# Kernel optimization log

Measured on AMD Instinct MI355X. Metric: run time of the kernel, lower is better.

Reference implementation:

```python
import jax, jax.numpy as jnp
import numpy as np
import math

NEIGHBOR_RADIUS = 30.0

def _masked_softmax(logits, mask, axis):
    # mask: bool, True = keep; all-masked rows return zeros
    p = jax.nn.softmax(jnp.where(mask, logits, -1e9), axis=axis) * mask.astype(logits.dtype)
    return p / jnp.clip(jnp.sum(p, axis=axis, keepdims=True), 1e-9, None)

def _forward(agents_state, agents_mask, map_polylines, map_poly_mask,
             map_poly_type, map_tl_status, map_on_route,
             pm_w1, pm_b1, pm_w2, pm_b2, type_emb, tl_emb, route_emb,
             mo_w1, mo_b1, mo_w2, mo_b2,
             ae_w1, ae_b1, ae_w2, ae_b2, ae_w3, ae_b3,
             mr_w1, mr_b1, mr_w2, mr_b2,
             nr_w1, nr_b1, nr_w2, nr_b2,
             to_w1, to_b1, to_w2, to_b2):
    relu = jax.nn.relu
    a_mask = (agents_mask > 0.5).astype(agents_state.dtype)   # (B,N,T)
    a_feat = agents_state[..., :5]
    # ---- map polyline node encoder ----
    h = relu(map_polylines @ pm_w1 + pm_b1)                   # (B,M,L,H)
    h = relu(h @ pm_w2 + pm_b2)
    h = h.max(axis=2)                                         # (B,M,H) max-pool over points
    t_idx = jnp.clip(map_poly_type, 0, type_emb.shape[0] - 1)
    s_idx = jnp.clip(map_tl_status, 0, tl_emb.shape[0] - 1)
    r_idx = jnp.clip(map_on_route, 0, route_emb.shape[0] - 1)
    h = h + type_emb[t_idx] + tl_emb[s_idx] + route_emb[r_idx]
    h = relu(h @ mo_w1 + mo_b1) @ mo_w2 + mo_b2
    map_mask = map_poly_mask > 0.5                            # (B,M) bool
    map_node = h * map_mask[..., None].astype(h.dtype)        # (B,M,D)
    map_center = map_polylines.mean(axis=2)                   # (B,M,2)
    # ---- agent state encoder ----
    a = relu(a_feat @ ae_w1 + ae_b1)
    a = relu(a @ ae_w2 + ae_b2)
    a_emb = (a @ ae_w3 + ae_b3) * a_mask[..., None]           # (B,N,T,D)
    D = a_emb.shape[-1]
    # ---- agent -> map attention ----
    agent_pos = a_feat[..., 0:2]
    rel = map_center[:, None, None, :, :] - agent_pos[:, :, :, None, :]  # (B,N,T,M,2)
    dist = jnp.linalg.norm(rel, axis=-1, keepdims=True)
    rel_feat = jnp.concatenate([rel, dist], axis=-1)          # (B,N,T,M,3)
    rel_score = (relu(rel_feat @ mr_w1 + mr_b1) @ mr_w2 + mr_b2)[..., 0]  # (B,N,T,M)
    dot = jnp.einsum('bntd,bmd->bntm', a_emb, map_node) / math.sqrt(D)
    score_mask = jnp.broadcast_to(map_mask[:, None, None, :], dot.shape)
    attn = _masked_softmax(dot + rel_score, score_mask, axis=-1)
    map_ctx = jnp.einsum('bntm,bmd->bntd', attn, map_node)    # (B,N,T,D)
    # ---- neighbor graph attention ----
    pos = a_feat[..., 0:2]
    vel = a_feat[..., 3:5]
    pos_j = jnp.transpose(pos, (0, 2, 1, 3))                  # (B,T,N,2)
    vel_j = jnp.transpose(vel, (0, 2, 1, 3))
    rel_pos = pos_j[:, None, :, :, :] - pos[:, :, :, None, :] # (B,N,T,N,2) = p_j - p_i
    rel_vel = vel_j[:, None, :, :, :] - vel[:, :, :, None, :]
    dist_ij = jnp.linalg.norm(rel_pos, axis=-1, keepdims=True)
    rel_ij = jnp.concatenate([rel_pos, rel_vel, dist_ij], axis=-1)        # (B,N,T,N,5)
    nbr_score = (relu(rel_ij @ nr_w1 + nr_b1) @ nr_w2 + nr_b2)[..., 0]    # (B,N,T,N)
    am_b = agents_mask > 0.5
    valid_i = am_b[..., None]                                 # (B,N,T,1)
    valid_j = jnp.transpose(am_b, (0, 2, 1))[:, None, :, :]   # (B,1,T,N)
    N = pos.shape[1]
    not_self = ~jnp.eye(N, dtype=bool)[None, :, None, :]      # (1,N,1,N)
    nbr_mask = valid_i & valid_j & (dist_ij[..., 0] <= NEIGHBOR_RADIUS) & not_self
    dot_n = jnp.einsum('bitd,bjtd->bitj', a_emb, a_emb) / math.sqrt(D)
    w_n = _masked_softmax(dot_n + nbr_score, nbr_mask, axis=-1)
    nbr_ctx = jnp.einsum('bitj,bjtd->bitd', w_n, a_emb)       # (B,N,T,D)
    # ---- tau head ----
    tau = jnp.concatenate([a_emb, map_ctx, nbr_ctx], axis=-1)
    tau = relu(tau @ to_w1 + to_b1) @ to_w2 + to_b2
    return tau * a_mask[..., None]

def setup_inputs() -> dict:
    key = jax.random.key(0)
    B, N, T, M, L = 2, 32, 32, 256, 20
    H, D, TAU = 128, 128, 64
    ks = jax.random.split(key, 32)
    def f(i, shp):
        return jax.random.normal(ks[i], shp, jnp.float32) * 0.05
    inp = {}
    inp['agents_state'] = jax.random.normal(ks[0], (B, N, T, 5), jnp.float32) * jnp.array([50., 50., 1., 5., 5.], jnp.float32)
    inp['agents_mask'] = jnp.ones((B, N, T), jnp.float32)
    inp['map_polylines'] = jax.random.normal(ks[1], (B, M, L, 2), jnp.float32) * 50.0
    inp['map_poly_mask'] = jnp.ones((B, M), jnp.float32)
    inp['map_poly_type'] = jax.random.randint(ks[2], (B, M), 0, 4)
    inp['map_tl_status'] = jax.random.randint(ks[3], (B, M), 0, 8)
    inp['map_on_route'] = jax.random.randint(ks[4], (B, M), 0, 2)
    inp['pm_w1'] = f(5, (2, H));  inp['pm_b1'] = jnp.zeros((H,), jnp.float32)
    inp['pm_w2'] = f(6, (H, H)); inp['pm_b2'] = jnp.zeros((H,), jnp.float32)
    inp['type_emb'] = f(7, (4, H)); inp['tl_emb'] = f(8, (8, H)); inp['route_emb'] = f(9, (2, H))
    inp['mo_w1'] = f(10, (H, H)); inp['mo_b1'] = jnp.zeros((H,), jnp.float32)
    inp['mo_w2'] = f(11, (H, D)); inp['mo_b2'] = jnp.zeros((D,), jnp.float32)
    inp['ae_w1'] = f(12, (5, H)); inp['ae_b1'] = jnp.zeros((H,), jnp.float32)
    inp['ae_w2'] = f(13, (H, H)); inp['ae_b2'] = jnp.zeros((H,), jnp.float32)
    inp['ae_w3'] = f(14, (H, D)); inp['ae_b3'] = jnp.zeros((D,), jnp.float32)
    inp['mr_w1'] = f(15, (3, H)); inp['mr_b1'] = jnp.zeros((H,), jnp.float32)
    inp['mr_w2'] = f(16, (H, 1)); inp['mr_b2'] = jnp.zeros((1,), jnp.float32)
    inp['nr_w1'] = f(17, (5, H)); inp['nr_b1'] = jnp.zeros((H,), jnp.float32)
    inp['nr_w2'] = f(18, (H, 1)); inp['nr_b2'] = jnp.zeros((1,), jnp.float32)
    inp['to_w1'] = f(19, (3 * D, H)); inp['to_b1'] = jnp.zeros((H,), jnp.float32)
    inp['to_w2'] = f(20, (H, TAU)); inp['to_b2'] = jnp.zeros((TAU,), jnp.float32)
    return inp

def reference(agents_state, agents_mask, map_polylines, map_poly_mask,
              map_poly_type, map_tl_status, map_on_route,
              pm_w1, pm_b1, pm_w2, pm_b2, type_emb, tl_emb, route_emb,
              mo_w1, mo_b1, mo_w2, mo_b2,
              ae_w1, ae_b1, ae_w2, ae_b2, ae_w3, ae_b3,
              mr_w1, mr_b1, mr_w2, mr_b2,
              nr_w1, nr_b1, nr_w2, nr_b2,
              to_w1, to_b1, to_w2, to_b2):
    return _forward(agents_state, agents_mask, map_polylines, map_poly_mask,
                    map_poly_type, map_tl_status, map_on_route,
                    pm_w1, pm_b1, pm_w2, pm_b2, type_emb, tl_emb, route_emb,
                    mo_w1, mo_b1, mo_w2, mo_b2,
                    ae_w1, ae_b1, ae_w2, ae_b2, ae_w3, ae_b3,
                    mr_w1, mr_b1, mr_w2, mr_b2,
                    nr_w1, nr_b1, nr_w2, nr_b2,
                    to_w1, to_b1, to_w2, to_b2)
```

## Files before the change

kernel.cpp:

```cpp
#include <hip/hip_runtime.h>

#define RSQRT_D 0.08838834764831843f

__global__ __launch_bounds__(256) void kAB_front(
    const float* __restrict__ poly, const float* __restrict__ pmask,
    const int* __restrict__ ptype, const int* __restrict__ ptl, const int* __restrict__ proute,
    const float* __restrict__ pm_w1, const float* __restrict__ pm_b1,
    const float* __restrict__ pm_w2, const float* __restrict__ pm_b2,
    const float* __restrict__ type_emb, const float* __restrict__ tl_emb, const float* __restrict__ route_emb,
    const float* __restrict__ mo_w1, const float* __restrict__ mo_b1,
    const float* __restrict__ mo_w2, const float* __restrict__ mo_b2,
    const float* __restrict__ astate, const float* __restrict__ amask,
    const float* __restrict__ ae_w1, const float* __restrict__ ae_b1,
    const float* __restrict__ ae_w2, const float* __restrict__ ae_b2,
    const float* __restrict__ ae_w3, const float* __restrict__ ae_b3,
    float* __restrict__ map_node, float* __restrict__ map_nodeT, float* __restrict__ center,
    float* __restrict__ a_emb, float* __restrict__ aT, float* __restrict__ posT)
{
    int tid = threadIdx.x;
    if (blockIdx.x < 512) {
        int bm = blockIdx.x;
        int b = bm >> 8, m = bm & 255;
        int h = tid & 127, rw = tid >> 7;
        __shared__ float xch[2][128];
        __shared__ __align__(16) float hvs[128];
        __shared__ __align__(16) float g2[128];
        __shared__ __align__(16) float h1s[2][128][12];

        {
            int k = h;
            int half = rw;
            const float* pp = poly + bm*40 + half*20;
            float wx = pm_w1[k], wy = pm_w1[128+k], bb = pm_b1[k];
            float h1v[10];
            #pragma unroll
            for (int u = 0; u < 10; ++u) {
                float x = pp[2*u], y = pp[2*u+1];
                h1v[u] = fmaxf(fmaf(wx, x, fmaf(wy, y, bb)), 0.f);
            }
            float4 s0 = make_float4(h1v[0], h1v[1], h1v[2], h1v[3]);
            float4 s1 = make_float4(h1v[4], h1v[5], h1v[6], h1v[7]);
            float2 s2 = make_float2(h1v[8], h1v[9]);
            *(float4*)&h1s[half][k][0] = s0;
            *(float4*)&h1s[half][k][4] = s1;
            *(float2*)&h1s[half][k][8] = s2;
        }
        __syncthreads();

        float acc[10];
        #pragma unroll
        for (int u = 0; u < 10; ++u) acc[u] = 0.f;
        const float* w2p = pm_w2 + h;
        #pragma unroll 2
        for (int k = 0; k < 128; ++k) {
            float w2v = w2p[k*128];
            float4 A  = *(const float4*)&h1s[rw][k][0];
            float4 Bv = *(const float4*)&h1s[rw][k][4];
            float2 Cv = *(const float2*)&h1s[rw][k][8];
            acc[0] = fmaf(A.x,  w2v, acc[0]);
            acc[1] = fmaf(A.y,  w2v, acc[1]);
            acc[2] = fmaf(A.z,  w2v, acc[2]);
            acc[3] = fmaf(A.w,  w2v, acc[3]);
            acc[4] = fmaf(Bv.x, w2v, acc[4]);
            acc[5] = fmaf(Bv.y, w2v, acc[5]);
            acc[6] = fmaf(Bv.z, w2v, acc[6]);
            acc[7] = fmaf(Bv.w, w2v, acc[7]);
            acc[8] = fmaf(Cv.x, w2v, acc[8]);
            acc[9] = fmaf(Cv.y, w2v, acc[9]);
        }
        float mx = acc[0];
        #pragma unroll
        for (int u = 1; u < 10; ++u) mx = fmaxf(mx, acc[u]);
        xch[rw][h] = mx;
        __syncthreads();
        if (rw == 0) {
            float v = fmaxf(fmaxf(mx, xch[1][h]) + pm_b2[h], 0.f);
            int ti = min(max(ptype[bm],0),3);
            int si = min(max(ptl[bm],0),7);
            int ri = min(max(proute[bm],0),1);
            hvs[h] = v + type_emb[ti*128+h] + tl_emb[si*128+h] + route_emb[ri*128+h];
        }
        __syncthreads();
        {
            float a1 = (rw == 0) ? mo_b1[h] : 0.f;
            int k0 = rw * 64;
            for (int kc = 0; kc < 16; ++kc) {
                float4 xv = *(const float4*)&hvs[k0 + kc*4];
                a1 = fmaf(xv.x, mo_w1[(k0+kc*4+0)*128+h],
                     fmaf(xv.y, mo_w1[(k0+kc*4+1)*128+h],
                     fmaf(xv.z, mo_w1[(k0+kc*4+2)*128+h],
                     fmaf(xv.w, mo_w1[(k0+kc*4+3)*128+h], a1))));
            }
            xch[rw][h] = a1;
        }
        __syncthreads();
        if (tid < 128) g2[tid] = fmaxf(xch[0][tid] + xch[1][tid], 0.f);
        __syncthreads();
        {
            float a2 = (rw == 0) ? mo_b2[h] : 0.f;
            int k0 = rw * 64;
            for (int kc = 0; kc < 16; ++kc) {
                float4 xv = *(const float4*)&g2[k0 + kc*4];
                a2 = fmaf(xv.x, mo_w2[(k0+kc*4+0)*128+h],
                     fmaf(xv.y, mo_w2[(k0+kc*4+1)*128+h],
                     fmaf(xv.z, mo_w2[(k0+kc*4+2)*128+h],
                     fmaf(xv.w, mo_w2[(k0+kc*4+3)*128+h], a2))));
            }
            xch[rw][h] = a2;
        }
        __syncthreads();
        if (tid < 128) {
            float a2 = xch[0][tid] + xch[1][tid];
            float mk = (pmask[bm] > 0.5f) ? 1.f : 0.f;
            a2 *= mk;
            map_node[bm*128 + tid] = a2;
            map_nodeT[(b*128+tid)*256 + m] = a2;
        }
        if (tid == 0) {
            float sx = 0.f, sy = 0.f;
            #pragma unroll
            for (int l = 0; l < 20; ++l) { sx += poly[bm*40 + 2*l]; sy += poly[bm*40 + 2*l + 1]; }
            center[bm*2+0] = sx * 0.05f;
            center[bm*2+1] = sy * 0.05f;
        }
    } else {
        int h = tid & 127, rp = tid >> 7;
        int r0 = (blockIdx.x - 512)*8 + rp*4;
        __shared__ float f5[2][4][5];
        __shared__ __align__(16) float a1s[2][4][128];
        if (h < 20) f5[rp][h/5][h%5] = astate[(r0 + h/5)*5 + (h%5)];
        __syncthreads();
        float b1v = ae_b1[h];
        float v[4];
        {
            float w0 = ae_w1[h], w1 = ae_w1[128+h], w2 = ae_w1[256+h], w3 = ae_w1[384+h], w4 = ae_w1[512+h];
            #pragma unroll
            for (int r = 0; r < 4; ++r) {
                float a = b1v;
                a = fmaf(f5[rp][r][0], w0, a); a = fmaf(f5[rp][r][1], w1, a);
                a = fmaf(f5[rp][r][2], w2, a); a = fmaf(f5[rp][r][3], w3, a);
                a = fmaf(f5[rp][r][4], w4, a);
                v[r] = fmaxf(a, 0.f);
            }
        }
        #pragma unroll
        for (int r = 0; r < 4; ++r) a1s[rp][r][h] = v[r];
        __syncthreads();
        {
            float b2v = ae_b2[h];
            float a0 = b2v, a1 = b2v, a2 = b2v, a3 = b2v;
            for (int kc = 0; kc < 32; ++kc) {
                float4 x0 = *(const float4*)&a1s[rp][0][kc*4];
                float4 x1 = *(const float4*)&a1s[rp][1][kc*4];
                float4 x2 = *(const float4*)&a1s[rp][2][kc*4];
                float4 x3 = *(const float4*)&a1s[rp][3][kc*4];
                float w0 = ae_w2[(kc*4+0)*128+h], w1 = ae_w2[(kc*4+1)*128+h];
                float w2 = ae_w2[(kc*4+2)*128+h], w3 = ae_w2[(kc*4+3)*128+h];
                a0 = fmaf(x0.x,w0,fmaf(x0.y,w1,fmaf(x0.z,w2,fmaf(x0.w,w3,a0))));
                a1 = fmaf(x1.x,w0,fmaf(x1.y,w1,fmaf(x1.z,w2,fmaf(x1.w,w3,a1))));
                a2 = fmaf(x2.x,w0,fmaf(x2.y,w1,fmaf(x2.z,w2,fmaf(x2.w,w3,a2))));
                a3 = fmaf(x3.x,w0,fmaf(x3.y,w1,fmaf(x3.z,w2,fmaf(x3.w,w3,a3))));
            }
            v[0]=fmaxf(a0,0.f); v[1]=fmaxf(a1,0.f); v[2]=fmaxf(a2,0.f); v[3]=fmaxf(a3,0.f);
        }
        __syncthreads();
        #pragma unroll
        for (int r = 0; r < 4; ++r) a1s[rp][r][h] = v[r];
        __syncthreads();
        {
            float b3v = ae_b3[h];
            float a0 = b3v, a1 = b3v, a2 = b3v, a3 = b3v;
            for (int kc = 0; kc < 32; ++kc) {
                float4 x0 = *(const float4*)&a1s[rp][0][kc*4];
                float4 x1 = *(const float4*)&a1s[rp][1][kc*4];
                float4 x2 = *(const float4*)&a1s[rp][2][kc*4];
                float4 x3 = *(const float4*)&a1s[rp][3][kc*4];
                float w0 = ae_w3[(kc*4+0)*128+h], w1 = ae_w3[(kc*4+1)*128+h];
                float w2 = ae_w3[(kc*4+2)*128+h], w3 = ae_w3[(kc*4+3)*128+h];
                a0 = fmaf(x0.x,w0,fmaf(x0.y,w1,fmaf(x0.z,w2,fmaf(x0.w,w3,a0))));
                a1 = fmaf(x1.x,w0,fmaf(x1.y,w1,fmaf(x1.z,w2,fmaf(x1.w,w3,a1))));
                a2 = fmaf(x2.x,w0,fmaf(x2.y,w1,fmaf(x2.z,w2,fmaf(x2.w,w3,a2))));
                a3 = fmaf(x3.x,w0,fmaf(x3.y,w1,fmaf(x3.z,w2,fmaf(x3.w,w3,a3))));
            }
            v[0]=a0; v[1]=a1; v[2]=a2; v[3]=a3;
        }
        #pragma unroll
        for (int r = 0; r < 4; ++r) {
            int rr = r0 + r;
            float mk = (amask[rr] > 0.5f) ? 1.f : 0.f;
            float e = v[r] * mk;
            a_emb[rr*128 + h] = e;
            int bb = rr >> 10, nn = (rr >> 5) & 31, tt = rr & 31;
            int bt = bb*32 + tt;
            aT[(bt*128 + h)*32 + nn] = e;
        }
        if (h < 20) {
            int r = h / 5, c = h % 5;
            int rr = r0 + r;
            int bb = rr >> 10, nn = (rr >> 5) & 31, tt = rr & 31;
            int bt = bb*32 + tt;
            float val;
            if      (c == 0) val = f5[rp][r][0];
            else if (c == 1) val = f5[rp][r][1];
            else if (c == 2) val = f5[rp][r][3];
            else if (c == 3) val = f5[rp][r][4];
            else             val = amask[rr];
            posT[(bt*5 + c)*32 + nn] = val;
        }
    }
}

__global__ __launch_bounds__(512) void kCD_fused(
    const float* __restrict__ astate, const float* __restrict__ amask,
    const float* __restrict__ pmask,
    const float* __restrict__ a_emb, const float* __restrict__ map_node,
    const float* __restrict__ map_nodeT, const float* __restrict__ center,
    const float* __restrict__ mr_w1, const float* __restrict__ mr_b1,
    const float* __restrict__ mr_w2, const float* __restrict__ mr_b2,
    const float* __restrict__ aT, const float* __restrict__ posT,
    const float* __restrict__ nr_w1, const float* __restrict__ nr_b1,
    const float* __restrict__ nr_w2, const float* __restrict__ nr_b2,
    const float* __restrict__ to_w1, const float* __restrict__ to_b1,
    const float* __restrict__ to_w2, const float* __restrict__ to_b2,
    float* __restrict__ out)
{
    int tid = threadIdx.x;
    int r0 = blockIdx.x * 4;
    int b = r0 >> 10, t0 = r0 & 31;

    __shared__ float lg4[4][256];
    __shared__ __align__(16) float p4[256*4];
    __shared__ float ctxp[4][128];
    __shared__ float pj[4][32];
    __shared__ __align__(16) float tau[4][384];
    __shared__ float redn[4][128];
    __shared__ __align__(16) float gpart[4][4][128];
    __shared__ __align__(16) float g1s[4][128];

    if (tid < 256) {
        int m = tid;
        float rx[4], ry[4], dd[4], dt[4], sA[4];
        float b2c = mr_b2[0];
        float cx = center[(b*256+m)*2+0], cy = center[(b*256+m)*2+1];
        #pragma unroll
        for (int r = 0; r < 4; ++r) {
            float px = astate[(r0+r)*5+0], py = astate[(r0+r)*5+1];
            rx[r] = cx - px; ry[r] = cy - py;
            dd[r] = sqrtf(rx[r]*rx[r] + ry[r]*ry[r]);
            dt[r] = 0.f; sA[r] = b2c;
        }
        const float* mT = map_nodeT + b*128*256 + m;
        const float* ae0 = a_emb + (size_t)(r0+0)*128;
        const float* ae1 = a_emb + (size_t)(r0+1)*128;
        const float* ae2 = a_emb + (size_t)(r0+2)*128;
        const float* ae3 = a_emb + (size_t)(r0+3)*128;
        #pragma unroll 4
        for (int hh = 0; hh < 128; ++hh) {
            float wa = mr_w1[hh], wb = mr_w1[128+hh], wc = mr_w1[256+hh];
            float bb = mr_b1[hh], w2 = mr_w2[hh];
            float v = mT[hh*256];
            float t10 = fmaf(rx[0], wa, fmaf(ry[0], wb, fmaf(dd[0], wc, bb)));
            float t11 = fmaf(rx[1], wa, fmaf(ry[1], wb, fmaf(dd[1], wc, bb)));
            float t12 = fmaf(rx[2], wa, fmaf(ry[2], wb, fmaf(dd[2], wc, bb)));
            float t13 = fmaf(rx[3], wa, fmaf(ry[3], wb, fmaf(dd[3], wc, bb)));
            sA[0] = fmaf(fmaxf(t10, 0.f), w2, sA[0]);
            sA[1] = fmaf(fmaxf(t11, 0.f), w2, sA[1]);
            sA[2] = fmaf(fmaxf(t12, 0.f), w2, sA[2]);
            sA[3] = fmaf(fmaxf(t13, 0.f), w2, sA[3]);
            dt[0] = fmaf(v, ae0[hh], dt[0]);
            dt[1] = fmaf(v, ae1[hh], dt[1]);
            dt[2] = fmaf(v, ae2[hh], dt[2]);
            dt[3] = fmaf(v, ae3[hh], dt[3]);
        }
        bool mk = pmask[b*256+m] > 0.5f;
        #pragma unroll
        for (int r = 0; r < 4; ++r)
            lg4[r][m] = mk ? fmaf(dt[r], RSQRT_D, sA[r]) : -1e30f;
    } else {
        int lam = tid & 63, wv = (tid >> 6) & 3;
        int r = r0 + wv;
        int ii = (r >> 5) & 31, tt = r & 31;
        int bt = b*32 + tt;
        int j = lam & 31, hs = lam >> 5;
        float pxi = astate[r*5+0], pyi = astate[r*5+1], vxi = astate[r*5+3], vyi = astate[r*5+4];
        const float* pT = posT + bt*160;
        float pxj = pT[j], pyj = pT[32+j], vxj = pT[64+j], vyj = pT[96+j], mj = pT[128+j];
        float rpx = pxj-pxi, rpy = pyj-pyi, rvx = vxj-vxi, rvy = vyj-vyi;
        float ddv = sqrtf(rpx*rpx + rpy*rpy);
        const float* ei = a_emb + (size_t)r*128;
        const float* aTp = aT + (size_t)bt*4096 + j;
        float s = 0.f, dot = 0.f;
        int h0 = hs*64;
        #pragma unroll 8
        for (int q = 0; q < 64; ++q) {
            int hh = h0 + q;
            float wA = nr_w1[hh], wB = nr_w1[128+hh], wC = nr_w1[256+hh];
            float wD = nr_w1[384+hh], wE = nr_w1[512+hh];
            float bb = nr_b1[hh], w2 = nr_w2[hh];
            float t1 = fmaf(rpx, wA, fmaf(rpy, wB, fmaf(rvx, wC,
                       fmaf(rvy, wD, fmaf(ddv, wE, bb)))));
            s = fmaf(fmaxf(t1, 0.f), w2, s);
            dot = fmaf(ei[hh], aTp[hh*32], dot);
        }
        s   += __shfl_xor(s, 32);
        dot += __shfl_xor(dot, 32);
        bool vi = amask[r] > 0.5f, vj = mj > 0.5f;
        bool ok = vi && vj && (ddv <= 30.0f) && (j != ii);
        float lg = ok ? fmaf(dot, RSQRT_D, s + nr_b2[0]) : -1e30f;
        float mxv = lg;
        #pragma unroll
        for (int off = 16; off; off >>= 1) mxv = fmaxf(mxv, __shfl_xor(mxv, off));
        float e = (lg > -1e29f) ? expf(lg - mxv) : 0.f;
        float sm = e;
        #pragma unroll
        for (int off = 16; off; off >>= 1) sm += __shfl_xor(sm, off);
        if (hs == 0) pj[wv][j] = e / fmaxf(sm, 1e-9f);
    }
    __syncthreads();

    if (tid < 256) {
        int lam = tid & 63, wv = tid >> 6;
        float x0 = lg4[wv][lam], x1 = lg4[wv][64+lam], x2 = lg4[wv][128+lam], x3 = lg4[wv][192+lam];
        float mxv = fmaxf(fmaxf(x0,x1), fmaxf(x2,x3));
        #pragma unroll
        for (int off = 32; off; off >>= 1) mxv = fmaxf(mxv, __shfl_xor(mxv, off));
        float e0 = (x0 > -1e29f) ? expf(x0-mxv) : 0.f;
        float e1 = (x1 > -1e29f) ? expf(x1-mxv) : 0.f;
        float e2 = (x2 > -1e29f) ? expf(x2-mxv) : 0.f;
        float e3 = (x3 > -1e29f) ? expf(x3-mxv) : 0.f;
        float sm = e0+e1+e2+e3;
        #pragma unroll
        for (int off = 32; off; off >>= 1) sm += __shfl_xor(sm, off);
        float inv = 1.f / fmaxf(sm, 1e-9f);
        p4[lam*4 + wv]       = e0*inv;
        p4[(64+lam)*4 + wv]  = e1*inv;
        p4[(128+lam)*4 + wv] = e2*inv;
        p4[(192+lam)*4 + wv] = e3*inv;
    } else {
        int idx = tid - 256;
        int d = idx & 127, rr = idx >> 7;
        tau[rr][d]   = a_emb[(size_t)(r0+rr)*128 + d];
        tau[rr+2][d] = a_emb[(size_t)(r0+rr+2)*128 + d];
    }
    __syncthreads();

    float pv0 = 0.f, pv1 = 0.f, pv2 = 0.f, pv3 = 0.f;
    float na0 = 0.f, na1 = 0.f, na2 = 0.f, na3 = 0.f;
    if (tid < 256) {
        int d = tid & 127, hf = tid >> 7;
        const float* mn = map_node + (b*256 + hf*128)*128 + d;
        const float4* ppv = (const float4*)p4 + hf*128;
        #pragma unroll 4
        for (int mm = 0; mm < 128; ++mm) {
            float4 pvv = ppv[mm];
            float v = mn[mm*128];
            pv0 = fmaf(pvv.x, v, pv0); pv1 = fmaf(pvv.y, v, pv1);
            pv2 = fmaf(pvv.z, v, pv2); pv3 = fmaf(pvv.w, v, pv3);
        }
        if (hf == 1) { ctxp[0][d]=pv0; ctxp[1][d]=pv1; ctxp[2][d]=pv2; ctxp[3][d]=pv3; }
    } else {
        int local = tid - 256;
        int d = local & 127, hf = local >> 7;
        for (int jj = 0; jj < 16; ++jj) {
            int j2 = hf*16 + jj;
            float p0 = pj[0][j2], p1 = pj[1][j2], p2 = pj[2][j2], p3 = pj[3][j2];
            const float* ejb = a_emb + (size_t)((b*32 + j2)*32 + t0)*128 + d;
            na0 = fmaf(p0, ejb[0],   na0);
            na1 = fmaf(p1, ejb[128], na1);
            na2 = fmaf(p2, ejb[256], na2);
            na3 = fmaf(p3, ejb[384], na3);
        }
        if (hf == 1) { redn[0][d]=na0; redn[1][d]=na1; redn[2][d]=na2; redn[3][d]=na3; }
    }
    __syncthreads();

    if (tid < 128) {
        int d = tid;
        tau[0][128+d] = pv0 + ctxp[0][d];
        tau[1][128+d] = pv1 + ctxp[1][d];
        tau[2][128+d] = pv2 + ctxp[2][d];
        tau[3][128+d] = pv3 + ctxp[3][d];
    } else if (tid >= 256 && tid < 384) {
        int d = tid - 256;
        tau[0][256+d] = na0 + redn[0][d];
        tau[1][256+d] = na1 + redn[1][d];
        tau[2][256+d] = na2 + redn[2][d];
        tau[3][256+d] = na3 + redn[3][d];
    }
    __syncthreads();

    {
        int h6 = tid & 63, kq = (tid >> 6) & 3, side = tid >> 8;
        int col = side*64 + h6;
        float a0v = 0.f, a1v = 0.f, a2v = 0.f, a3v = 0.f;
        for (int c = 0; c < 24; ++c) {
            int k4 = kq*24 + c;
            float4 x0 = *(const float4*)&tau[0][k4*4];
            float4 x1 = *(const float4*)&tau[1][k4*4];
            float4 x2 = *(const float4*)&tau[2][k4*4];
            float4 x3 = *(const float4*)&tau[3][k4*4];
            float w0 = to_w1[(k4*4+0)*128 + col];
            float w1 = to_w1[(k4*4+1)*128 + col];
            float w2 = to_w1[(k4*4+2)*128 + col];
            float w3 = to_w1[(k4*4+3)*128 + col];
            a0v = fmaf(x0.x,w0,fmaf(x0.y,w1,fmaf(x0.z,w2,fmaf(x0.w,w3,a0v))));
            a1v = fmaf(x1.x,w0,fmaf(x1.y,w1,fmaf(x1.z,w2,fmaf(x1.w,w3,a1v))));
            a2v = fmaf(x2.x,w0,fmaf(x2.y,w1,fmaf(x2.z,w2,fmaf(x2.w,w3,a2v))));
            a3v = fmaf(x3.x,w0,fmaf(x3.y,w1,fmaf(x3.z,w2,fmaf(x3.w,w3,a3v))));
        }
        gpart[kq][0][col] = a0v;
        gpart[kq][1][col] = a1v;
        gpart[kq][2][col] = a2v;
        gpart[kq][3][col] = a3v;
    }
    __syncthreads();

    {
        int h = tid & 127, rr = tid >> 7;
        float s = gpart[0][rr][h] + gpart[1][rr][h] + gpart[2][rr][h] + gpart[3][rr][h];
        g1s[rr][h] = fmaxf(s + to_b1[h], 0.f);
    }
    __syncthreads();

    if (tid < 256) {
        int o = tid & 63, row = tid >> 6;
        float a2 = to_b2[o];
        for (int kc = 0; kc < 32; ++kc) {
            float4 g = *(const float4*)&g1s[row][kc*4];
            a2 = fmaf(g.x, to_w2[(kc*4+0)*64 + o],
                 fmaf(g.y, to_w2[(kc*4+1)*64 + o],
                 fmaf(g.z, to_w2[(kc*4+2)*64 + o],
                 fmaf(g.w, to_w2[(kc*4+3)*64 + o], a2))));
        }
        float mk = (amask[r0+row] > 0.5f) ? 1.f : 0.f;
        out[(r0+row)*64 + o] = a2 * mk;
    }
}

extern "C" void kernel_launch(void* const* d_in, const int* in_sizes, int n_in,
                              void* d_out, int out_size, void* d_ws, size_t ws_size,
                              hipStream_t stream) {
    const float* agents_state  = (const float*)d_in[0];
    const float* agents_mask   = (const float*)d_in[1];
    const float* map_polylines = (const float*)d_in[2];
    const float* map_poly_mask = (const float*)d_in[3];
    const int*   map_poly_type = (const int*)d_in[4];
    const int*   map_tl_status = (const int*)d_in[5];
    const int*   map_on_route  = (const int*)d_in[6];
    const float* pm_w1 = (const float*)d_in[7];
    const float* pm_b1 = (const float*)d_in[8];
    const float* pm_w2 = (const float*)d_in[9];
    const float* pm_b2 = (const float*)d_in[10];
    const float* type_emb  = (const float*)d_in[11];
    const float* tl_emb    = (const float*)d_in[12];
    const float* route_emb = (const float*)d_in[13];
    const float* mo_w1 = (const float*)d_in[14];
    const float* mo_b1 = (const float*)d_in[15];
    const float* mo_w2 = (const float*)d_in[16];
    const float* mo_b2 = (const float*)d_in[17];
    const float* ae_w1 = (const float*)d_in[18];
    const float* ae_b1 = (const float*)d_in[19];
    const float* ae_w2 = (const float*)d_in[20];
    const float* ae_b2 = (const float*)d_in[21];
    const float* ae_w3 = (const float*)d_in[22];
    const float* ae_b3 = (const float*)d_in[23];
    const float* mr_w1 = (const float*)d_in[24];
    const float* mr_b1 = (const float*)d_in[25];
    const float* mr_w2 = (const float*)d_in[26];
    const float* mr_b2 = (const float*)d_in[27];
    const float* nr_w1 = (const float*)d_in[28];
    const float* nr_b1 = (const float*)d_in[29];
    const float* nr_w2 = (const float*)d_in[30];
    const float* nr_b2 = (const float*)d_in[31];
    const float* to_w1 = (const float*)d_in[32];
    const float* to_b1 = (const float*)d_in[33];
    const float* to_w2 = (const float*)d_in[34];
    const float* to_b2 = (const float*)d_in[35];

    float* ws = (float*)d_ws;
    float* map_node  = ws;
    float* map_nodeT = ws + 65536;
    float* center    = ws + 131072;
    float* a_emb     = ws + 132096;
    float* aT        = ws + 394240;
    float* posT      = ws + 656384;

    float* out = (float*)d_out;

    kAB_front<<<768, 256, 0, stream>>>(map_polylines, map_poly_mask,
        map_poly_type, map_tl_status, map_on_route,
        pm_w1, pm_b1, pm_w2, pm_b2, type_emb, tl_emb, route_emb,
        mo_w1, mo_b1, mo_w2, mo_b2,
        agents_state, agents_mask,
        ae_w1, ae_b1, ae_w2, ae_b2, ae_w3, ae_b3,
        map_node, map_nodeT, center, a_emb, aT, posT);

    kCD_fused<<<512, 512, 0, stream>>>(agents_state, agents_mask, map_poly_mask,
        a_emb, map_node, map_nodeT, center,
        mr_w1, mr_b1, mr_w2, mr_b2,
        aT, posT,
        nr_w1, nr_b1, nr_w2, nr_b2,
        to_w1, to_b1, to_w2, to_b2,
        out);
}
```

Before: 179.5 us.

## Halve rows per block in fused attention kernel and split map-score reduction

Each block of the fused agent-map/agent-agent/output kernel now handles 2 rows instead of 4, and the grid is doubled to 1024 blocks. The map-logit loop over 128 hidden units is split across two thread halves, whose partial sums are combined through shared memory. The a_emb load is moved into the otherwise idle threads of the first phase, and launch bounds now request 8 waves per SIMD. This raises parallelism and occupancy, at the cost of weight reuse across rows, so to_w1, map_node and the MLP weights are re-read twice as often.

```diff
diff --git a/kernel.cpp b/kernel.cpp
--- a/kernel.cpp
+++ b/kernel.cpp
@@ -210,7 +210,7 @@
     }
 }
 
-__global__ __launch_bounds__(512) void kCD_fused(
+__global__ __launch_bounds__(512, 8) void kCD_fused(
     const float* __restrict__ astate, const float* __restrict__ amask,
     const float* __restrict__ pmask,
     const float* __restrict__ a_emb, const float* __restrict__ map_node,
@@ -225,59 +225,61 @@
     float* __restrict__ out)
 {
     int tid = threadIdx.x;
-    int r0 = blockIdx.x * 4;
+    int r0 = blockIdx.x * 2;
     int b = r0 >> 10, t0 = r0 & 31;
 
-    __shared__ float lg4[4][256];
-    __shared__ __align__(16) float p4[256*4];
-    __shared__ float ctxp[4][128];
-    __shared__ float pj[4][32];
-    __shared__ __align__(16) float tau[4][384];
-    __shared__ float redn[4][128];
-    __shared__ __align__(16) float gpart[4][4][128];
-    __shared__ __align__(16) float g1s[4][128];
-
-    if (tid < 256) {
-        int m = tid;
-        float rx[4], ry[4], dd[4], dt[4], sA[4];
+    __shared__ float lg4[2][256];
+    __shared__ __align__(16) float p4[256*2];
+    __shared__ float sp1[2][256];
+    __shared__ float dp1[2][256];
+    __shared__ float ctxp[2][128];
+    __shared__ float pj[2][32];
+    __shared__ __align__(16) float tau[2][384];
+    __shared__ float redn[2][128];
+    __shared__ __align__(16) float gpart[4][2][128];
+    __shared__ __align__(16) float g1s[2][128];
+
+    float sA0, sA1, dt0, dt1;
+    {
+        int m = tid & 255, kh = tid >> 8;
         float b2c = mr_b2[0];
         float cx = center[(b*256+m)*2+0], cy = center[(b*256+m)*2+1];
-        #pragma unroll
-        for (int r = 0; r < 4; ++r) {
-            float px = astate[(r0+r)*5+0], py = astate[(r0+r)*5+1];
-            rx[r] = cx - px; ry[r] = cy - py;
-            dd[r] = sqrtf(rx[r]*rx[r] + ry[r]*ry[r]);
-            dt[r] = 0.f; sA[r] = b2c;
-        }
+        float px0 = astate[(r0+0)*5+0], py0 = astate[(r0+0)*5+1];
+        float px1 = astate[(r0+1)*5+0], py1 = astate[(r0+1)*5+1];
+        float rx0 = cx - px0, ry0 = cy - py0;
+        float rx1 = cx - px1, ry1 = cy - py1;
+        float dd0 = sqrtf(rx0*rx0 + ry0*ry0);
+        float dd1 = sqrtf(rx1*rx1 + ry1*ry1);
+        sA0 = kh ? 0.f : b2c; sA1 = sA0;
+        dt0 = 0.f; dt1 = 0.f;
         const float* mT = map_nodeT + b*128*256 + m;
         const float* ae0 = a_emb + (size_t)(r0+0)*128;
         const float* ae1 = a_emb + (size_t)(r0+1)*128;
-        const float* ae2 = a_emb + (size_t)(r0+2)*128;
-        const float* ae3 = a_emb + (size_t)(r0+3)*128;
+        int h0 = kh*64;
         #pragma unroll 4
-        for (int hh = 0; hh < 128; ++hh) {
+        for (int q = 0; q < 64; ++q) {
+            int hh = h0 + q;
             float wa = mr_w1[hh], wb = mr_w1[128+hh], wc = mr_w1[256+hh];
             float bb = mr_b1[hh], w2 = mr_w2[hh];
             float v = mT[hh*256];
-            float t10 = fmaf(rx[0], wa, fmaf(ry[0], wb, fmaf(dd[0], wc, bb)));
-            float t11 = fmaf(rx[1], wa, fmaf(ry[1], wb, fmaf(dd[1], wc, bb)));
-            float t12 = fmaf(rx[2], wa, fmaf(ry[2], wb, fmaf(dd[2], wc, bb)));
-            float t13 = fmaf(rx[3], wa, fmaf(ry[3], wb, fmaf(dd[3], wc, bb)));
-            sA[0] = fmaf(fmaxf(t10, 0.f), w2, sA[0]);
-            sA[1] = fmaf(fmaxf(t11, 0.f), w2, sA[1]);
-            sA[2] = fmaf(fmaxf(t12, 0.f), w2, sA[2]);
-            sA[3] = fmaf(fmaxf(t13, 0.f), w2, sA[3]);
-            dt[0] = fmaf(v, ae0[hh], dt[0]);
-            dt[1] = fmaf(v, ae1[hh], dt[1]);
-            dt[2] = fmaf(v, ae2[hh], dt[2]);
-            dt[3] = fmaf(v, ae3[hh], dt[3]);
-        }
+            float t10 = fmaf(rx0, wa, fmaf(ry0, wb, fmaf(dd0, wc, bb)));
+            float t11 = fmaf(rx1, wa, fmaf(ry1, wb, fmaf(dd1, wc, bb)));
+            sA0 = fmaf(fmaxf(t10, 0.f), w2, sA0);
+            sA1 = fmaf(fmaxf(t11, 0.f), w2, sA1);
+            dt0 = fmaf(v, ae0[hh], dt0);
+            dt1 = fmaf(v, ae1[hh], dt1);
+        }
+        if (kh) { sp1[0][m] = sA0; sp1[1][m] = sA1; dp1[0][m] = dt0; dp1[1][m] = dt1; }
+    }
+    __syncthreads();
+
+    if (tid < 256) {
+        int m = tid;
         bool mk = pmask[b*256+m] > 0.5f;
-        #pragma unroll
-        for (int r = 0; r < 4; ++r)
-            lg4[r][m] = mk ? fmaf(dt[r], RSQRT_D, sA[r]) : -1e30f;
-    } else {
-        int lam = tid & 63, wv = (tid >> 6) & 3;
+        lg4[0][m] = mk ? fmaf(dt0 + dp1[0][m], RSQRT_D, sA0 + sp1[0][m]) : -1e30f;
+        lg4[1][m] = mk ? fmaf(dt1 + dp1[1][m], RSQRT_D, sA1 + sp1[1][m]) : -1e30f;
+    } else if (tid < 384) {
+        int lam = tid & 63, wv = (tid >> 6) & 1;
         int r = r0 + wv;
         int ii = (r >> 5) & 31, tt = r & 31;
         int bt = b*32 + tt;
@@ -315,10 +317,14 @@
         #pragma unroll
         for (int off = 16; off; off >>= 1) sm += __shfl_xor(sm, off);
         if (hs == 0) pj[wv][j] = e / fmaxf(sm, 1e-9f);
-    }
-    __syncthreads();
-
-    if (tid < 256) {
+    } else {
+        int d = tid & 127;
+        tau[0][d] = a_emb[(size_t)r0*128 + d];
+        tau[1][d] = a_emb[(size_t)(r0+1)*128 + d];
+    }
+    __syncthreads();
+
+    if (tid < 128) {
         int lam = tid & 63, wv = tid >> 6;
         float x0 = lg4[wv][lam], x1 = lg4[wv][64+lam], x2 = lg4[wv][128+lam], x3 = lg4[wv][192+lam];
         float mxv = fmaxf(fmaxf(x0,x1), fmaxf(x2,x3));
@@ -332,45 +338,37 @@
         #pragma unroll
         for (int off = 32; off; off >>= 1) sm += __shfl_xor(sm, off);
         float inv = 1.f / fmaxf(sm, 1e-9f);
-        p4[lam*4 + wv]       = e0*inv;
-        p4[(64+lam)*4 + wv]  = e1*inv;
-        p4[(128+lam)*4 + wv] = e2*inv;
-        p4[(192+lam)*4 + wv] = e3*inv;
-    } else {
-        int idx = tid - 256;
-        int d = idx & 127, rr = idx >> 7;
-        tau[rr][d]   = a_emb[(size_t)(r0+rr)*128 + d];
-        tau[rr+2][d] = a_emb[(size_t)(r0+rr+2)*128 + d];
-    }
-    __syncthreads();
-
-    float pv0 = 0.f, pv1 = 0.f, pv2 = 0.f, pv3 = 0.f;
-    float na0 = 0.f, na1 = 0.f, na2 = 0.f, na3 = 0.f;
+        p4[lam*2 + wv]       = e0*inv;
+        p4[(64+lam)*2 + wv]  = e1*inv;
+        p4[(128+lam)*2 + wv] = e2*inv;
+        p4[(192+lam)*2 + wv] = e3*inv;
+    }
+    __syncthreads();
+
+    float pv0 = 0.f, pv1 = 0.f;
+    float na0 = 0.f, na1 = 0.f;
     if (tid < 256) {
         int d = tid & 127, hf = tid >> 7;
         const float* mn = map_node + (b*256 + hf*128)*128 + d;
-        const float4* ppv = (const float4*)p4 + hf*128;
-        #pragma unroll 4
+        const float2* ppv = (const float2*)p4 + hf*128;
+        #pragma unroll 8
         for (int mm = 0; mm < 128; ++mm) {
-            float4 pvv = ppv[mm];
+            float2 pvv = ppv[mm];
             float v = mn[mm*128];
             pv0 = fmaf(pvv.x, v, pv0); pv1 = fmaf(pvv.y, v, pv1);
-            pv2 = fmaf(pvv.z, v, pv2); pv3 = fmaf(pvv.w, v, pv3);
-        }
-        if (hf == 1) { ctxp[0][d]=pv0; ctxp[1][d]=pv1; ctxp[2][d]=pv2; ctxp[3][d]=pv3; }
+        }
+        if (hf == 1) { ctxp[0][d]=pv0; ctxp[1][d]=pv1; }
     } else {
         int local = tid - 256;
         int d = local & 127, hf = local >> 7;
         for (int jj = 0; jj < 16; ++jj) {
             int j2 = hf*16 + jj;
-            float p0 = pj[0][j2], p1 = pj[1][j2], p2 = pj[2][j2], p3 = pj[3][j2];
+            float p0 = pj[0][j2], p1 = pj[1][j2];
             const float* ejb = a_emb + (size_t)((b*32 + j2)*32 + t0)*128 + d;
             na0 = fmaf(p0, ejb[0],   na0);
             na1 = fmaf(p1, ejb[128], na1);
-            na2 = fmaf(p2, ejb[256], na2);
-            na3 = fmaf(p3, ejb[384], na3);
-        }
-        if (hf == 1) { redn[0][d]=na0; redn[1][d]=na1; redn[2][d]=na2; redn[3][d]=na3; }
+        }
+        if (hf == 1) { redn[0][d]=na0; redn[1][d]=na1; }
     }
     __syncthreads();
 
@@ -378,51 +376,41 @@
         int d = tid;
         tau[0][128+d] = pv0 + ctxp[0][d];
         tau[1][128+d] = pv1 + ctxp[1][d];
-        tau[2][128+d] = pv2 + ctxp[2][d];
-        tau[3][128+d] = pv3 + ctxp[3][d];
     } else if (tid >= 256 && tid < 384) {
         int d = tid - 256;
         tau[0][256+d] = na0 + redn[0][d];
         tau[1][256+d] = na1 + redn[1][d];
-        tau[2][256+d] = na2 + redn[2][d];
-        tau[3][256+d] = na3 + redn[3][d];
     }
     __syncthreads();
 
     {
         int h6 = tid & 63, kq = (tid >> 6) & 3, side = tid >> 8;
         int col = side*64 + h6;
-        float a0v = 0.f, a1v = 0.f, a2v = 0.f, a3v = 0.f;
+        float a0v = 0.f, a1v = 0.f;
         for (int c = 0; c < 24; ++c) {
             int k4 = kq*24 + c;
             float4 x0 = *(const float4*)&tau[0][k4*4];
             float4 x1 = *(const float4*)&tau[1][k4*4];
-            float4 x2 = *(const float4*)&tau[2][k4*4];
-            float4 x3 = *(const float4*)&tau[3][k4*4];
             float w0 = to_w1[(k4*4+0)*128 + col];
             float w1 = to_w1[(k4*4+1)*128 + col];
             float w2 = to_w1[(k4*4+2)*128 + col];
             float w3 = to_w1[(k4*4+3)*128 + col];
             a0v = fmaf(x0.x,w0,fmaf(x0.y,w1,fmaf(x0.z,w2,fmaf(x0.w,w3,a0v))));
             a1v = fmaf(x1.x,w0,fmaf(x1.y,w1,fmaf(x1.z,w2,fmaf(x1.w,w3,a1v))));
-            a2v = fmaf(x2.x,w0,fmaf(x2.y,w1,fmaf(x2.z,w2,fmaf(x2.w,w3,a2v))));
-            a3v = fmaf(x3.x,w0,fmaf(x3.y,w1,fmaf(x3.z,w2,fmaf(x3.w,w3,a3v))));
         }
         gpart[kq][0][col] = a0v;
         gpart[kq][1][col] = a1v;
-        gpart[kq][2][col] = a2v;
-        gpart[kq][3][col] = a3v;
-    }
-    __syncthreads();
-
-    {
+    }
+    __syncthreads();
+
+    if (tid < 256) {
         int h = tid & 127, rr = tid >> 7;
         float s = gpart[0][rr][h] + gpart[1][rr][h] + gpart[2][rr][h] + gpart[3][rr][h];
         g1s[rr][h] = fmaxf(s + to_b1[h], 0.f);
     }
     __syncthreads();
 
-    if (tid < 256) {
+    if (tid < 128) {
         int o = tid & 63, row = tid >> 6;
         float a2 = to_b2[o];
         for (int kc = 0; kc < 32; ++kc) {
@@ -495,7 +483,7 @@
         ae_w1, ae_b1, ae_w2, ae_b2, ae_w3, ae_b3,
         map_node, map_nodeT, center, a_emb, aT, posT);
 
-    kCD_fused<<<512, 512, 0, stream>>>(agents_state, agents_mask, map_poly_mask,
+    kCD_fused<<<1024, 512, 0, stream>>>(agents_state, agents_mask, map_poly_mask,
         a_emb, map_node, map_nodeT, center,
         mr_w1, mr_b1, mr_w2, mr_b2,
         aT, posT,
```

New measurement: 211.0 us. 17.6% more time.
